# Kernel tuning notes

Hardware: AMD Instinct MI355X
Metric: run time of the kernel (lower is better)

Reference implementation:

```python
import jax, jax.numpy as jnp
import numpy as np

B, N, A, M, H, KD, VD, O = 256, 2048, 256, 256, 8, 32, 32, 256
EPS = 1e-10

def setup_inputs() -> dict:
    key = jax.random.key(0)
    ks = jax.random.split(key, 8)
    return {
        "q_data": jax.random.normal(ks[0], (B, N, A), dtype=jnp.float32),
        "m_data": jax.random.normal(ks[1], (B, N, M), dtype=jnp.float32),
        "q_mask": jnp.ones((B, N, 1), dtype=jnp.float32),
        "bias": jnp.zeros((B, 1, N), dtype=jnp.float32),
        "query_w": 0.02 * jax.random.normal(ks[2], (A, H, KD), dtype=jnp.float32),
        "key_w": 0.02 * jax.random.normal(ks[3], (M, KD), dtype=jnp.float32),
        "value_w": 0.02 * jax.random.normal(ks[4], (M, VD), dtype=jnp.float32),
        "gating_w": 0.02 * jax.random.normal(ks[5], (A, H, VD), dtype=jnp.float32),
        "gating_b": jnp.zeros((H, VD), dtype=jnp.float32),
        "output_w": 0.02 * jax.random.normal(ks[6], (H, VD, O), dtype=jnp.float32),
        "output_b": jnp.zeros((O,), dtype=jnp.float32),
    }

def reference(q_data, m_data, q_mask, bias, query_w, key_w, value_w,
              gating_w, gating_b, output_w, output_b):
    # masked mean over the query axis: q_mask [B,N,1] broadcasts over channels
    q_avg = jnp.sum(q_mask * q_data, axis=1) / (jnp.sum(q_mask, axis=1) + EPS)  # [B,A]
    kd = query_w.shape[-1]
    q = jnp.einsum('ba,ahc->bhc', q_avg, query_w) * kd ** (-0.5)  # [B,H,KD]
    k = jnp.einsum('bka,ac->bkc', m_data, key_w)                  # [B,N,KD]
    v = jnp.einsum('bka,ac->bkc', m_data, value_w)                # [B,N,VD]
    # the incoming `bias` arg is overwritten by the module, as in the original
    attn_bias = 1e9 * (q_mask[:, None, :, 0] - 1.0)               # [B,1,N]
    logits = jnp.einsum('bhc,bkc->bhk', q, k) + attn_bias         # [B,H,N]
    weights = jax.nn.softmax(logits, axis=-1)
    weighted_avg = jnp.einsum('bhk,bkc->bhc', weights, v)         # [B,H,VD]
    # gating == True
    gate = jax.nn.sigmoid(jnp.einsum('bqc,chv->bqhv', q_data, gating_w) + gating_b)
    gated = weighted_avg[:, None] * gate                          # [B,N,H,VD]
    out = jnp.einsum('bqhc,hco->bqo', gated, output_w) + output_b # [B,N,O]
    return out
```

## Files before the change

### kernel.cpp

```cpp
#include <hip/hip_runtime.h>

#define B_ 256
#define N_ 2048
#define A_ 256
#define M_ 256
#define H_ 8
#define KD_ 32
#define VD_ 32
#define O_ 256

typedef float f32x4 __attribute__((ext_vector_type(4)));
typedef __bf16 bf16x8 __attribute__((ext_vector_type(8)));
typedef unsigned short u16x8 __attribute__((ext_vector_type(8)));

union FragU { u16x8 u; bf16x8 b; };

__device__ __forceinline__ unsigned short f2bf(float f) {
  union { __bf16 b; unsigned short u; } c;
  c.b = (__bf16)f;
  return c.u;
}
__device__ __forceinline__ float bf2f(unsigned short h) {
  return __uint_as_float(((unsigned int)h) << 16);
}

__device__ __forceinline__ void gll16(const void* gsrc, void* ldst) {
  __builtin_amdgcn_global_load_lds(
      (const __attribute__((address_space(1))) void*)gsrc,
      (__attribute__((address_space(3))) void*)ldst, 16, 0, 0);
}

__global__ void pack_weights(const float* __restrict__ gating_w,
                             const float* __restrict__ output_w,
                             const float* __restrict__ key_w,
                             const float* __restrict__ value_w,
                             unsigned short* __restrict__ wg,
                             unsigned short* __restrict__ wo,
                             unsigned short* __restrict__ wkv) {
  int idx = blockIdx.x * 256 + threadIdx.x;
  int j = idx & 7;
  int lane = (idx >> 3) & 63;
  int rest = idx >> 9;
  int kc = rest & 7, ct = rest >> 3;
  int row = kc * 32 + ((lane >> 4) << 3) + j;
  int col = ct * 16 + (lane & 15);
  wg[idx] = f2bf(gating_w[row * 256 + col]);
  wo[idx] = f2bf(output_w[row * 256 + col]);
  if (idx < 16384) {
    float v = (col < 32) ? key_w[row * 32 + col] : value_w[row * 32 + (col - 32)];
    wkv[idx] = f2bf(v);
  }
}

__global__ void reduce_q(const float* __restrict__ qd, const float* __restrict__ qm,
                         const float* __restrict__ qw, float* __restrict__ q_out) {
  int b = blockIdx.x;
  int t = threadIdx.x;
  int l = t & 63, g = t >> 6;
  const float* qdb = qd + (size_t)b * N_ * A_;
  const float* qmb = qm + (size_t)b * N_;
  f32x4 sum = {0.f, 0.f, 0.f, 0.f};
  float msum = 0.f;
  for (int n = g; n < N_; n += 16) {
    float m = qmb[n];
    msum += m;
    f32x4 v = *(const f32x4*)(qdb + (size_t)n * A_ + l * 4);
    sum += m * v;
  }
  __shared__ float s[16][256];
  __shared__ float ms[16];
  __shared__ float qavg[256];
  *(f32x4*)&s[g][l * 4] = sum;
  if (l == 0) ms[g] = msum;
  __syncthreads();
  if (t < 256) {
    float tot = 0.f;
#pragma unroll
    for (int k = 0; k < 16; k++) tot += s[k][t];
    float mt = 0.f;
#pragma unroll
    for (int k = 0; k < 16; k++) mt += ms[k];
    qavg[t] = tot / (mt + 1e-10f);
  }
  __syncthreads();
  if (t < 256) {
    float acc = 0.f;
    for (int a2 = 0; a2 < 256; a2++) acc += qavg[a2] * qw[a2 * 256 + t];
    q_out[b * 256 + t] = acc * 0.17677669529663687f;
  }
}

__global__ void kv_gemm(const float* __restrict__ md,
                        const unsigned short* __restrict__ wkv,
                        unsigned short* __restrict__ k_ws,
                        unsigned short* __restrict__ v_ws) {
  int t = threadIdx.x;
  int w = t >> 6, l = t & 63, q = l >> 4, l15 = l & 15;
  size_t r0 = (size_t)blockIdx.x * 128;
  int b = (int)(r0 >> 11);
  int n0 = (int)(r0 & 2047);
  f32x4 acc[2][4] = {};
  for (int kc = 0; kc < 8; kc++) {
    FragU bfr[4];
#pragma unroll
    for (int ct = 0; ct < 4; ct++)
      bfr[ct].u = *(const u16x8*)(wkv + (((ct * 8 + kc) * 64 + l) << 3));
    FragU af[2];
#pragma unroll
    for (int rt = 0; rt < 2; rt++) {
      size_t row = r0 + (size_t)(w * 32 + rt * 16 + l15);
      const float4* s4 = (const float4*)(md + row * 256 + kc * 32 + q * 8);
      float4 u0 = s4[0], u1 = s4[1];
      af[rt].u = (u16x8){f2bf(u0.x), f2bf(u0.y), f2bf(u0.z), f2bf(u0.w),
                         f2bf(u1.x), f2bf(u1.y), f2bf(u1.z), f2bf(u1.w)};
    }
#pragma unroll
    for (int ct = 0; ct < 4; ct++) {
      acc[0][ct] = __builtin_amdgcn_mfma_f32_16x16x32_bf16(af[0].b, bfr[ct].b, acc[0][ct], 0, 0, 0);
      acc[1][ct] = __builtin_amdgcn_mfma_f32_16x16x32_bf16(af[1].b, bfr[ct].b, acc[1][ct], 0, 0, 0);
    }
  }
#pragma unroll
  for (int rt = 0; rt < 2; rt++)
#pragma unroll
    for (int ct = 0; ct < 4; ct++)
#pragma unroll
      for (int r = 0; r < 4; r++) {
        int rloc = w * 32 + rt * 16 + q * 4 + r;
        if (ct < 2) {
          k_ws[(r0 + rloc) * 32 + ct * 16 + l15] = f2bf(acc[rt][ct][r]);
        } else {
          v_ws[((size_t)b * 32 + (ct - 2) * 16 + l15) * N_ + (n0 + rloc)] = f2bf(acc[rt][ct][r]);
        }
      }
}

__global__ void attn_softmax(const unsigned short* __restrict__ k_ws,
                             const unsigned short* __restrict__ v_ws,
                             const float* __restrict__ qv,
                             const float* __restrict__ qm,
                             float* __restrict__ wa) {
  int b = blockIdx.x, t = threadIdx.x;
  __shared__ float lg[8][2048];
  __shared__ float red[4][256];
  __shared__ float inv_s[8];
  const float* qb = qv + b * 256;
  const float* qmb = qm + (size_t)b * N_;
  for (int n = t; n < N_; n += 1024) {
    const u16x8* kr = (const u16x8*)(k_ws + ((size_t)(b * N_ + n)) * 32);
    u16x8 ka = kr[0], kb2 = kr[1], kc2 = kr[2], kd2 = kr[3];
    float kf[32];
#pragma unroll
    for (int j = 0; j < 8; j++) {
      kf[j]      = bf2f(ka[j]);
      kf[8 + j]  = bf2f(kb2[j]);
      kf[16 + j] = bf2f(kc2[j]);
      kf[24 + j] = bf2f(kd2[j]);
    }
    float bias_n = 1e9f * (qmb[n] - 1.0f);
#pragma unroll
    for (int h = 0; h < 8; h++) {
      float d = 0.f;
#pragma unroll
      for (int c = 0; c < 32; c++) d += qb[h * 32 + c] * kf[c];
      lg[h][n] = d + bias_n;
    }
  }
  __syncthreads();
  if (t < 256) {
    int h = t >> 5, i = t & 31;
    float m = -3.0e38f;
    for (int n = i; n < N_; n += 32) m = fmaxf(m, lg[h][n]);
#pragma unroll
    for (int off = 16; off; off >>= 1) m = fmaxf(m, __shfl_xor(m, off));
    float s = 0.f;
    for (int n = i; n < N_; n += 32) {
      float e = __expf(lg[h][n] - m);
      lg[h][n] = e;
      s += e;
    }
#pragma unroll
    for (int off = 16; off; off >>= 1) s += __shfl_xor(s, off);
    if (i == 0) inv_s[h] = 1.0f / s;
  }
  __syncthreads();
  {
    int c = t & 31, h = (t >> 5) & 7, nq = t >> 8;
    const u16x8* vb = (const u16x8*)(v_ws + ((size_t)b * 32 + c) * N_ + nq * 512);
    const f32x4* lg4 = (const f32x4*)&lg[h][nq * 512];
    float acc = 0.f;
#pragma unroll 4
    for (int n8 = 0; n8 < 64; n8++) {
      u16x8 vv = vb[n8];
      f32x4 p0 = lg4[n8 * 2], p1 = lg4[n8 * 2 + 1];
      acc += p0[0] * bf2f(vv[0]);
      acc += p0[1] * bf2f(vv[1]);
      acc += p0[2] * bf2f(vv[2]);
      acc += p0[3] * bf2f(vv[3]);
      acc += p1[0] * bf2f(vv[4]);
      acc += p1[1] * bf2f(vv[5]);
      acc += p1[2] * bf2f(vv[6]);
      acc += p1[3] * bf2f(vv[7]);
    }
    red[nq][t & 255] = acc;
  }
  __syncthreads();
  if (t < 256) {
    float r = red[0][t] + red[1][t] + red[2][t] + red[3][t];
    wa[b * 256 + t] = r * inv_s[t >> 5];
  }
}

__launch_bounds__(256, 2)
__global__ void gate_out(const float* __restrict__ qd,
                         const unsigned short* __restrict__ wg,
                         const unsigned short* __restrict__ wo,
                         const float* __restrict__ wa,
                         const float* __restrict__ gb,
                         const float* __restrict__ ob,
                         float* __restrict__ out) {
  int blk = blockIdx.x;
  int b = blk >> 4, tile = blk & 15;
  int t = threadIdx.x;
  int w = t >> 6, l = t & 63, q = l >> 4, l15 = l & 15;
  __shared__ __attribute__((aligned(16))) unsigned short wsg[8192];
  __shared__ __attribute__((aligned(16))) unsigned short wso[8192];
  __shared__ __attribute__((aligned(16))) unsigned short Pt[4][2][16][40];
  __shared__ float wa_s[256], gb_s[256], ob_s[256];
  wa_s[t] = wa[b * 256 + t];
  gb_s[t] = gb[t];
  ob_s[t] = ob[t];
  size_t rowbase = (size_t)b * N_ + tile * 128;

  {
    const char* wgb = (const char*)wg;
    const char* wob = (const char*)wo;
#pragma unroll
    for (int i = 0; i < 4; i++) {
      int ch = i * 4 + w;
      gll16(wgb + ch * 1024 + l * 16, (char*)wsg + ch * 1024);
      gll16(wob + ch * 8192 + l * 16, (char*)wso + ch * 1024);
    }
  }

  FragU af[2][8];
#pragma unroll
  for (int rt = 0; rt < 2; rt++) {
    const float* src = qd + (rowbase + (size_t)(w * 32 + rt * 16 + l15)) * 256 + q * 8;
#pragma unroll
    for (int kc = 0; kc < 8; kc++) {
      float4 u0 = *(const float4*)(src + kc * 32);
      float4 u1 = *(const float4*)(src + kc * 32 + 4);
      af[rt][kc].u = (u16x8){f2bf(u0.x), f2bf(u0.y), f2bf(u0.z), f2bf(u0.w),
                             f2bf(u1.x), f2bf(u1.y), f2bf(u1.z), f2bf(u1.w)};
    }
  }
  f32x4 acc[2][16] = {};
  __syncthreads();

  for (int g = 0; g < 8; g++) {
    f32x4 gacc[2][2] = {};
#pragma unroll
    for (int kc = 0; kc < 8; kc++) {
      FragU b0, b1;
      b0.u = *(const u16x8*)(wsg + (kc * 64 + l) * 8);
      b1.u = *(const u16x8*)(wsg + ((8 + kc) * 64 + l) * 8);
      gacc[0][0] = __builtin_amdgcn_mfma_f32_16x16x32_bf16(af[0][kc].b, b0.b, gacc[0][0], 0, 0, 0);
      gacc[0][1] = __builtin_amdgcn_mfma_f32_16x16x32_bf16(af[0][kc].b, b1.b, gacc[0][1], 0, 0, 0);
      gacc[1][0] = __builtin_amdgcn_mfma_f32_16x16x32_bf16(af[1][kc].b, b0.b, gacc[1][0], 0, 0, 0);
      gacc[1][1] = __builtin_amdgcn_mfma_f32_16x16x32_bf16(af[1][kc].b, b1.b, gacc[1][1], 0, 0, 0);
    }
#pragma unroll
    for (int rt = 0; rt < 2; rt++)
#pragma unroll
      for (int ctl = 0; ctl < 2; ctl++) {
        int colg = ctl * 16 + l15;
        int col = g * 32 + colg;
        float wav = wa_s[col], gbv = gb_s[col];
#pragma unroll
        for (int r = 0; r < 4; r++) {
          float x = gacc[rt][ctl][r] + gbv;
          float gate = 1.0f / (1.0f + __expf(-x));
          Pt[w][rt][q * 4 + r][colg] = f2bf(wav * gate);
        }
      }
    FragU pf[2];
#pragma unroll
    for (int rt = 0; rt < 2; rt++)
      pf[rt].u = *(const u16x8*)&Pt[w][rt][l15][q * 8];

    __syncthreads();
    if (g < 7) {
      const char* wgb = (const char*)wg + (size_t)(g + 1) * 16384;
#pragma unroll
      for (int i = 0; i < 4; i++) {
        int ch = i * 4 + w;
        gll16(wgb + ch * 1024 + l * 16, (char*)wsg + ch * 1024);
      }
    }
#pragma unroll
    for (int ct = 0; ct < 16; ct++) {
      FragU bo;
      bo.u = *(const u16x8*)(wso + (ct * 64 + l) * 8);
      acc[0][ct] = __builtin_amdgcn_mfma_f32_16x16x32_bf16(pf[0].b, bo.b, acc[0][ct], 0, 0, 0);
      acc[1][ct] = __builtin_amdgcn_mfma_f32_16x16x32_bf16(pf[1].b, bo.b, acc[1][ct], 0, 0, 0);
    }
    __syncthreads();
    if (g < 7) {
      const char* wob = (const char*)wo + (size_t)(g + 1) * 1024;
#pragma unroll
      for (int i = 0; i < 4; i++) {
        int ch = i * 4 + w;
        gll16(wob + ch * 8192 + l * 16, (char*)wso + ch * 1024);
      }
    }
  }
#pragma unroll
  for (int rt = 0; rt < 2; rt++)
#pragma unroll
    for (int ct = 0; ct < 16; ct++) {
      int col = ct * 16 + l15;
      float obv = ob_s[col];
      size_t orow = (rowbase + (size_t)(w * 32 + rt * 16 + q * 4)) * 256 + col;
#pragma unroll
      for (int r = 0; r < 4; r++)
        out[orow + (size_t)r * 256] = acc[rt][ct][r] + obv;
    }
}

extern "C" void kernel_launch(void* const* d_in, const int* in_sizes, int n_in,
                              void* d_out, int out_size, void* d_ws, size_t ws_size,
                              hipStream_t stream) {
  const float* q_data   = (const float*)d_in[0];
  const float* m_data   = (const float*)d_in[1];
  const float* q_mask   = (const float*)d_in[2];
  const float* query_w  = (const float*)d_in[4];
  const float* key_w    = (const float*)d_in[5];
  const float* value_w  = (const float*)d_in[6];
  const float* gating_w = (const float*)d_in[7];
  const float* gating_b = (const float*)d_in[8];
  const float* output_w = (const float*)d_in[9];
  const float* output_b = (const float*)d_in[10];
  float* out = (float*)d_out;

  char* ws = (char*)d_ws;
  float* q_ws            = (float*)(ws);
  float* wa_ws           = (float*)(ws + (256 << 10));
  unsigned short* wg_ws  = (unsigned short*)(ws + (512 << 10));
  unsigned short* wo_ws  = (unsigned short*)(ws + (640 << 10));
  unsigned short* wkv_ws = (unsigned short*)(ws + (768 << 10));
  unsigned short* k_wsp  = (unsigned short*)(ws + (800 << 10));
  unsigned short* v_wsp  = (unsigned short*)(ws + (800 << 10) + ((size_t)32 << 20));

  pack_weights<<<256, 256, 0, stream>>>(gating_w, output_w, key_w, value_w,
                                        wg_ws, wo_ws, wkv_ws);
  reduce_q<<<B_, 1024, 0, stream>>>(q_data, q_mask, query_w, q_ws);
  kv_gemm<<<(B_ * N_) / 128, 256, 0, stream>>>(m_data, wkv_ws, k_wsp, v_wsp);
  attn_softmax<<<B_, 1024, 0, stream>>>(k_wsp, v_wsp, q_ws, q_mask, wa_ws);
  gate_out<<<(B_ * N_) / 128, 256, 0, stream>>>(q_data, wg_ws, wo_ws, wa_ws,
                                                gating_b, output_b, out);
}
```

Baseline: 1.458 ms.

## Split attention softmax across head pairs and vectorize V stores

The attention/softmax kernel now launches four blocks per batch, each handling two heads. This cuts shared memory per block and the serial per-head work, so more blocks can be resident across the CUs. The cost is that K is reread four times per batch. Separately, the kv_gemm epilogue packs four bf16 V values into a single 8-byte store instead of issuing four scalar strided stores.

```diff
diff --git a/kernel.cpp b/kernel.cpp
--- a/kernel.cpp
+++ b/kernel.cpp
@@ -12,6 +12,7 @@
 typedef float f32x4 __attribute__((ext_vector_type(4)));
 typedef __bf16 bf16x8 __attribute__((ext_vector_type(8)));
 typedef unsigned short u16x8 __attribute__((ext_vector_type(8)));
+typedef unsigned short u16x4 __attribute__((ext_vector_type(4)));
 
 union FragU { u16x8 u; bf16x8 b; };
 
@@ -121,18 +122,22 @@
     }
   }
 #pragma unroll
-  for (int rt = 0; rt < 2; rt++)
-#pragma unroll
-    for (int ct = 0; ct < 4; ct++)
+  for (int rt = 0; rt < 2; rt++) {
+#pragma unroll
+    for (int ct = 0; ct < 2; ct++)
 #pragma unroll
       for (int r = 0; r < 4; r++) {
         int rloc = w * 32 + rt * 16 + q * 4 + r;
-        if (ct < 2) {
-          k_ws[(r0 + rloc) * 32 + ct * 16 + l15] = f2bf(acc[rt][ct][r]);
-        } else {
-          v_ws[((size_t)b * 32 + (ct - 2) * 16 + l15) * N_ + (n0 + rloc)] = f2bf(acc[rt][ct][r]);
-        }
+        k_ws[(r0 + rloc) * 32 + ct * 16 + l15] = f2bf(acc[rt][ct][r]);
       }
+#pragma unroll
+    for (int ct = 2; ct < 4; ct++) {
+      int nbase = n0 + w * 32 + rt * 16 + q * 4;
+      u16x4 pv = {f2bf(acc[rt][ct][0]), f2bf(acc[rt][ct][1]),
+                  f2bf(acc[rt][ct][2]), f2bf(acc[rt][ct][3])};
+      *(u16x4*)&v_ws[((size_t)b * 32 + (ct - 2) * 16 + l15) * N_ + nbase] = pv;
+    }
+  }
 }
 
 __global__ void attn_softmax(const unsigned short* __restrict__ k_ws,
@@ -140,11 +145,13 @@
                              const float* __restrict__ qv,
                              const float* __restrict__ qm,
                              float* __restrict__ wa) {
-  int b = blockIdx.x, t = threadIdx.x;
-  __shared__ float lg[8][2048];
-  __shared__ float red[4][256];
-  __shared__ float inv_s[8];
-  const float* qb = qv + b * 256;
+  int blk = blockIdx.x;
+  int b = blk >> 2, h0 = (blk & 3) * 2;
+  int t = threadIdx.x;
+  __shared__ float lg[2][2048];
+  __shared__ float red[16][64];
+  __shared__ float inv_s[2];
+  const float* qb = qv + b * 256 + h0 * 32;
   const float* qmb = qm + (size_t)b * N_;
   for (int n = t; n < N_; n += 1024) {
     const u16x8* kr = (const u16x8*)(k_ws + ((size_t)(b * N_ + n)) * 32);
@@ -159,38 +166,38 @@
     }
     float bias_n = 1e9f * (qmb[n] - 1.0f);
 #pragma unroll
-    for (int h = 0; h < 8; h++) {
+    for (int hl = 0; hl < 2; hl++) {
       float d = 0.f;
 #pragma unroll
-      for (int c = 0; c < 32; c++) d += qb[h * 32 + c] * kf[c];
-      lg[h][n] = d + bias_n;
-    }
-  }
-  __syncthreads();
-  if (t < 256) {
-    int h = t >> 5, i = t & 31;
+      for (int c = 0; c < 32; c++) d += qb[hl * 32 + c] * kf[c];
+      lg[hl][n] = d + bias_n;
+    }
+  }
+  __syncthreads();
+  if (t < 64) {
+    int hl = t >> 5, i = t & 31;
     float m = -3.0e38f;
-    for (int n = i; n < N_; n += 32) m = fmaxf(m, lg[h][n]);
+    for (int n = i; n < N_; n += 32) m = fmaxf(m, lg[hl][n]);
 #pragma unroll
     for (int off = 16; off; off >>= 1) m = fmaxf(m, __shfl_xor(m, off));
     float s = 0.f;
     for (int n = i; n < N_; n += 32) {
-      float e = __expf(lg[h][n] - m);
-      lg[h][n] = e;
+      float e = __expf(lg[hl][n] - m);
+      lg[hl][n] = e;
       s += e;
     }
 #pragma unroll
     for (int off = 16; off; off >>= 1) s += __shfl_xor(s, off);
-    if (i == 0) inv_s[h] = 1.0f / s;
+    if (i == 0) inv_s[hl] = 1.0f / s;
   }
   __syncthreads();
   {
-    int c = t & 31, h = (t >> 5) & 7, nq = t >> 8;
-    const u16x8* vb = (const u16x8*)(v_ws + ((size_t)b * 32 + c) * N_ + nq * 512);
-    const f32x4* lg4 = (const f32x4*)&lg[h][nq * 512];
+    int c = t & 31, hl = (t >> 5) & 1, nq = t >> 6;
+    const u16x8* vb = (const u16x8*)(v_ws + ((size_t)b * 32 + c) * N_ + nq * 128);
+    const f32x4* lg4 = (const f32x4*)&lg[hl][nq * 128];
     float acc = 0.f;
-#pragma unroll 4
-    for (int n8 = 0; n8 < 64; n8++) {
+#pragma unroll
+    for (int n8 = 0; n8 < 16; n8++) {
       u16x8 vv = vb[n8];
       f32x4 p0 = lg4[n8 * 2], p1 = lg4[n8 * 2 + 1];
       acc += p0[0] * bf2f(vv[0]);
@@ -202,12 +209,14 @@
       acc += p1[2] * bf2f(vv[6]);
       acc += p1[3] * bf2f(vv[7]);
     }
-    red[nq][t & 255] = acc;
-  }
-  __syncthreads();
-  if (t < 256) {
-    float r = red[0][t] + red[1][t] + red[2][t] + red[3][t];
-    wa[b * 256 + t] = r * inv_s[t >> 5];
+    red[nq][t & 63] = acc;
+  }
+  __syncthreads();
+  if (t < 64) {
+    float r = 0.f;
+#pragma unroll
+    for (int k = 0; k < 16; k++) r += red[k][t];
+    wa[b * 256 + (h0 + (t >> 5)) * 32 + (t & 31)] = r * inv_s[t >> 5];
   }
 }
 
@@ -356,7 +365,7 @@
                                         wg_ws, wo_ws, wkv_ws);
   reduce_q<<<B_, 1024, 0, stream>>>(q_data, q_mask, query_w, q_ws);
   kv_gemm<<<(B_ * N_) / 128, 256, 0, stream>>>(m_data, wkv_ws, k_wsp, v_wsp);
-  attn_softmax<<<B_, 1024, 0, stream>>>(k_wsp, v_wsp, q_ws, q_mask, wa_ws);
+  attn_softmax<<<B_ * 4, 1024, 0, stream>>>(k_wsp, v_wsp, q_ws, q_mask, wa_ws);
   gate_out<<<(B_ * N_) / 128, 256, 0, stream>>>(q_data, wg_ws, wo_ws, wa_ws,
                                                 gating_b, output_b, out);
 }
```

After: 1.468 ms. No clear change (+0.7%).
